# Kernel optimization log

Hardware: AMD Instinct MI355X
Metric: run time of the kernel (lower is better)

Reference implementation:

```python
import jax, jax.numpy as jnp
import numpy as np

H = 128   # hidden_size
C = 80    # number of classes / per-class GRUs


def setup_inputs():
    key = jax.random.key(0)
    ks = jax.random.split(key, 16)
    lengths = np.array([100 + 4 * j for j in range(C)], dtype=np.int64)   # ragged segment sizes
    ucl = np.concatenate([np.zeros(1, np.int64), np.cumsum(lengths)])     # [C+1] boundaries
    N = int(ucl[-1])                                                      # 20640 total boxes
    r = jax.random.normal
    return {
        "boxes_feature": r(ks[0], (N, 1024), jnp.float32),
        "boxes_score": r(ks[1], (N, 32), jnp.float32),
        "boxes_box": r(ks[2], (N, 4), jnp.float32),
        "all_class_boxes_feature": r(ks[3], (N, 1024), jnp.float32),
        "all_class_boxes_score": r(ks[4], (N, 32), jnp.float32),
        "all_class_boxes_box": r(ks[5], (N, 32), jnp.float32),
        "all_class_boxes_origin_score": r(ks[6], (N, 32), jnp.float32),
        "unique_class": np.ones(C, dtype=np.int64),
        "unique_class_len": ucl,
        "appear_W": r(ks[7], (H, 1024), jnp.float32) / np.sqrt(1024.0).astype(np.float32),
        "appear_b": jnp.zeros((H,), jnp.float32),
        "feat_W": r(ks[8], (H, H + 96), jnp.float32) / np.sqrt(float(H + 96)).astype(np.float32),
        "feat_b": jnp.zeros((H,), jnp.float32),
        "gru_Wih": r(ks[9], (C, 2, 3 * H, H), jnp.float32) / np.sqrt(float(H)).astype(np.float32),
        "gru_Whh": r(ks[10], (C, 2, 3 * H, H), jnp.float32) / np.sqrt(float(H)).astype(np.float32),
        "gru_bih": r(ks[11], (C, 2, 3 * H), jnp.float32) * 0.01,
        "gru_bhh": r(ks[12], (C, 2, 3 * H), jnp.float32) * 0.01,
        "out_W": r(ks[13], (1, 2 * H), jnp.float32) / np.sqrt(2.0 * H).astype(np.float32),
        "out_b": jnp.zeros((1,), jnp.float32),
    }


def _forward(all_class_boxes_feature, all_class_boxes_score, all_class_boxes_box,
             all_class_boxes_origin_score, unique_class, unique_class_len,
             appear_W, appear_b, feat_W, feat_b,
             gru_Wih, gru_Whh, gru_bih, gru_bhh, out_W, out_b):
    # --- static ragged bookkeeping (int inputs are concrete numpy) ---
    ucl = np.asarray(unique_class_len)
    lengths = ucl[1:] - ucl[:-1]                                   # [C]
    starts = ucl[:-1]
    L = int(lengths.max())
    t = np.arange(L)
    mask = jnp.asarray(t[None, :] < lengths[:, None])              # [C,L] valid-position mask
    gidx = jnp.asarray(starts[:, None] + np.minimum(t[None, :], lengths[:, None] - 1))  # [C,L]
    ridx = jnp.asarray(np.clip(lengths[:, None] - 1 - t[None, :], 0, None))             # [C,L]

    # --- shared feature pipeline ---
    feat = jax.nn.relu(all_class_boxes_feature @ appear_W.T + appear_b)   # [N,H]
    allf = jnp.concatenate([feat, all_class_boxes_score, all_class_boxes_box,
                            all_class_boxes_origin_score], axis=1)        # [N,H+96]
    dec = jax.nn.relu(allf @ feat_W.T + feat_b)                           # [N,H]

    X = dec[gidx]                                                  # [C,L,H] padded per-class segments
    Xr = jnp.take_along_axis(X, ridx[:, :, None], axis=1)          # time-reversed within each length

    def run_dir(Xd, Wih, Whh, bih, bhh):
        # precompute input projections; scan only carries the hidden recurrence
        Xp = jnp.einsum('clh,cgh->clg', Xd, Wih) + bih[:, None, :]  # [C,L,3H]

        def per_class(xp, m, Whh_c, bhh_c):
            def step(h, inp):
                x_t, m_t = inp
                gh = Whh_c @ h + bhh_c
                r = jax.nn.sigmoid(x_t[:H] + gh[:H])                # PyTorch gate order r,z,n
                z = jax.nn.sigmoid(x_t[H:2 * H] + gh[H:2 * H])
                n = jnp.tanh(x_t[2 * H:] + r * gh[2 * H:])
                h2 = jnp.where(m_t, (1.0 - z) * n + z * h, h)
                return h2, h2
            _, out = jax.lax.scan(step, jnp.zeros((H,), xp.dtype), (xp, m))
            return out                                              # [L,H]
        return jax.vmap(per_class)(Xp, mask, Whh, bhh)              # [C,L,H]

    out_f = run_dir(X, gru_Wih[:, 0], gru_Whh[:, 0], gru_bih[:, 0], gru_bhh[:, 0])
    out_r = run_dir(Xr, gru_Wih[:, 1], gru_Whh[:, 1], gru_bih[:, 1], gru_bhh[:, 1])
    out_bd = jnp.take_along_axis(out_r, ridx[:, :, None], axis=1)   # un-reverse backward outputs
    Y = jnp.concatenate([out_f, out_bd], axis=-1)                   # [C,L,2H]

    # flatten valid positions back to the original box order (segments are contiguous)
    seg = jnp.asarray(np.repeat(np.arange(C), lengths))
    loc = jnp.asarray(np.concatenate([np.arange(int(l)) for l in lengths]))
    flat = Y[seg, loc]                                              # [N,2H]
    return jax.nn.sigmoid(flat @ out_W.T + out_b)[:, None, :]       # [N,1,1] like torch output


def reference(boxes_feature, boxes_score, boxes_box, all_class_boxes_feature,
              all_class_boxes_score, all_class_boxes_box, all_class_boxes_origin_score,
              unique_class, unique_class_len, appear_W, appear_b, feat_W, feat_b,
              gru_Wih, gru_Whh, gru_bih, gru_bhh, out_W, out_b):
    # boxes_feature/boxes_score/boxes_box are accepted but unused, as in the torch forward
    return _forward(all_class_boxes_feature, all_class_boxes_score, all_class_boxes_box,
                    all_class_boxes_origin_score, unique_class, unique_class_len,
                    appear_W, appear_b, feat_W, feat_b,
                    gru_Wih, gru_Whh, gru_bih, gru_bhh, out_W, out_b)
```

## Files before the change

### kernel.cpp

```cpp
#include <hip/hip_runtime.h>
#include <hip/hip_bf16.h>
#include <cstdint>


typedef _Float16 half2_t __attribute__((ext_vector_type(2)));
typedef _Float16 half8_t __attribute__((ext_vector_type(8)));

__global__ __launch_bounds__(256) void concat_kernel(
    const float* __restrict__ score, const float* __restrict__ box,
    const float* __restrict__ orig, float* __restrict__ allf, int N)
{
    int idx = blockIdx.x * 256 + threadIdx.x;
    int total = N * 96;
    if (idx >= total) return;
    int n = idx / 96, j = idx - n * 96;
    float v;
    if (j < 32)      v = score[(size_t)n * 32 + j];
    else if (j < 64) v = box  [(size_t)n * 32 + j - 32];
    else             v = orig [(size_t)n * 32 + j - 64];
    allf[(size_t)n * 224 + 128 + j] = v;
}

__global__ __launch_bounds__(256) void gemm128_kernel(
    const float* __restrict__ A, int lda,
    const float* __restrict__ B,
    const float* __restrict__ bias,
    float* __restrict__ Cc, int ldc,
    int N, int K, int do_relu)
{
    __shared__ __align__(16) float As[16][64];
    __shared__ __align__(16) float Bs[16][128];
    const int tid = threadIdx.x;
    const int tx = tid & 15, ty = tid >> 4;
    const int n0 = blockIdx.x * 64;
    const int arow = tid >> 2;

    float acc[4][8] = {};

    int ar = n0 + arow; if (ar > N - 1) ar = N - 1;
    const float* Aptr  = A + (size_t)ar * lda + (tid & 3) * 4;
    const int m0 = tid >> 2;
    const int kq4 = (tid & 3) * 4;
    const float* Bptr0 = B + (size_t)m0 * K + (tid & 3) * 4;
    const float* Bptr1 = Bptr0 + (size_t)64 * K;

    float4 av = *(const float4*)(Aptr);
    float4 b0 = *(const float4*)(Bptr0);
    float4 b1 = *(const float4*)(Bptr1);

    for (int kb = 0; kb < K; kb += 16) {
        __syncthreads();
        As[kq4 + 0][arow] = av.x;
        As[kq4 + 1][arow] = av.y;
        As[kq4 + 2][arow] = av.z;
        As[kq4 + 3][arow] = av.w;
        Bs[kq4 + 0][m0] = b0.x; Bs[kq4 + 1][m0] = b0.y;
        Bs[kq4 + 2][m0] = b0.z; Bs[kq4 + 3][m0] = b0.w;
        Bs[kq4 + 0][m0 + 64] = b1.x; Bs[kq4 + 1][m0 + 64] = b1.y;
        Bs[kq4 + 2][m0 + 64] = b1.z; Bs[kq4 + 3][m0 + 64] = b1.w;
        __syncthreads();
        if (kb + 16 < K) {
            av = *(const float4*)(Aptr + kb + 16);
            b0 = *(const float4*)(Bptr0 + kb + 16);
            b1 = *(const float4*)(Bptr1 + kb + 16);
        }
        #pragma unroll
        for (int kk = 0; kk < 16; kk++) {
            float4 a = *(const float4*)&As[kk][ty * 4];
            float4 p = *(const float4*)&Bs[kk][tx * 8];
            float4 q = *(const float4*)&Bs[kk][tx * 8 + 4];
            float av4[4] = {a.x, a.y, a.z, a.w};
            float bv[8]  = {p.x, p.y, p.z, p.w, q.x, q.y, q.z, q.w};
            #pragma unroll
            for (int i = 0; i < 4; i++)
                #pragma unroll
                for (int j = 0; j < 8; j++)
                    acc[i][j] = fmaf(av4[i], bv[j], acc[i][j]);
        }
    }

    #pragma unroll
    for (int i = 0; i < 4; i++) {
        int row = n0 + ty * 4 + i;
        if (row >= N) continue;
        float o[8];
        #pragma unroll
        for (int j = 0; j < 8; j++) {
            float v = acc[i][j] + bias[tx * 8 + j];
            if (do_relu) v = v > 0.f ? v : 0.f;
            o[j] = v;
        }
        float4* dst = (float4*)(Cc + (size_t)row * ldc + tx * 8);
        dst[0] = make_float4(o[0], o[1], o[2], o[3]);
        dst[1] = make_float4(o[4], o[5], o[6], o[7]);
    }
}

__global__ __launch_bounds__(256) void xp_kernel(
    const float* __restrict__ dec,
    const float* __restrict__ Wih,
    const float* __restrict__ bih,
    const int* __restrict__ ucl,
    float* __restrict__ xp,
    int N)
{
    const int c = blockIdx.x;
    const int tile = blockIdx.y;
    const int d  = blockIdx.z / 3;
    const int mt = blockIdx.z % 3;
    const int start = ucl[c];
    const int len = ucl[c + 1] - start;
    const int t0 = tile * 64;
    if (t0 >= len) return;

    __shared__ __align__(16) float As[16][64];
    __shared__ __align__(16) float Bs[16][128];
    const int tid = threadIdx.x;
    const int tx = tid & 15, ty = tid >> 4;
    const int arow = tid >> 2;

    int t = t0 + arow; if (t > len - 1) t = len - 1;
    int srow = start + (d ? (len - 1 - t) : t);
    const float* Aptr = dec + (size_t)srow * 128 + (tid & 3) * 4;

    const float* Bbase = Wih + ((size_t)(c * 2 + d) * 384 + mt * 128) * 128;
    const int m0 = tid >> 2;
    const int kq4 = (tid & 3) * 4;
    const float* Bptr0 = Bbase + (size_t)m0 * 128 + (tid & 3) * 4;
    const float* Bptr1 = Bptr0 + (size_t)64 * 128;

    float4 av = *(const float4*)(Aptr);
    float4 b0 = *(const float4*)(Bptr0);
    float4 b1 = *(const float4*)(Bptr1);

    float acc[4][8] = {};
    for (int kb = 0; kb < 128; kb += 16) {
        __syncthreads();
        As[kq4 + 0][arow] = av.x;
        As[kq4 + 1][arow] = av.y;
        As[kq4 + 2][arow] = av.z;
        As[kq4 + 3][arow] = av.w;
        Bs[kq4 + 0][m0] = b0.x; Bs[kq4 + 1][m0] = b0.y;
        Bs[kq4 + 2][m0] = b0.z; Bs[kq4 + 3][m0] = b0.w;
        Bs[kq4 + 0][m0 + 64] = b1.x; Bs[kq4 + 1][m0 + 64] = b1.y;
        Bs[kq4 + 2][m0 + 64] = b1.z; Bs[kq4 + 3][m0 + 64] = b1.w;
        __syncthreads();
        if (kb + 16 < 128) {
            av = *(const float4*)(Aptr + kb + 16);
            b0 = *(const float4*)(Bptr0 + kb + 16);
            b1 = *(const float4*)(Bptr1 + kb + 16);
        }
        #pragma unroll
        for (int kk = 0; kk < 16; kk++) {
            float4 a = *(const float4*)&As[kk][ty * 4];
            float4 p = *(const float4*)&Bs[kk][tx * 8];
            float4 q = *(const float4*)&Bs[kk][tx * 8 + 4];
            float av4[4] = {a.x, a.y, a.z, a.w};
            float bv[8]  = {p.x, p.y, p.z, p.w, q.x, q.y, q.z, q.w};
            #pragma unroll
            for (int i = 0; i < 4; i++)
                #pragma unroll
                for (int j = 0; j < 8; j++)
                    acc[i][j] = fmaf(av4[i], bv[j], acc[i][j]);
        }
    }

    const float* bias = bih + (size_t)(c * 2 + d) * 384 + mt * 128;
    #pragma unroll
    for (int i = 0; i < 4; i++) {
        int tt = t0 + ty * 4 + i;
        if (tt >= len) continue;
        float o[8];
        #pragma unroll
        for (int j = 0; j < 8; j++) o[j] = acc[i][j] + bias[tx * 8 + j];
        float4* dst = (float4*)(xp + ((size_t)d * N + start + tt) * 384 + mt * 128 + tx * 8);
        dst[0] = make_float4(o[0], o[1], o[2], o[3]);
        dst[1] = make_float4(o[4], o[5], o[6], o[7]);
    }
}

__global__ __launch_bounds__(128, 1) void gru_kernel(
    const float* __restrict__ xp,
    const float* __restrict__ Whh,
    const float* __restrict__ bhh,
    const int* __restrict__ ucl,
    float* __restrict__ outY,
    int N)
{
    const int c = blockIdx.x, d = blockIdx.y;
    const int start = ucl[c];
    const int len = ucl[c + 1] - start;
    const int g = threadIdx.x;

    const float* wbase = Whh + (size_t)(c * 2 + d) * 384 * 128;
    half2_t w0[64], w1[64], w2[64];
    {
        const float2* r0 = (const float2*)(wbase + (size_t)g * 128);
        const float2* r1 = (const float2*)(wbase + (size_t)(g + 128) * 128);
        const float2* r2 = (const float2*)(wbase + (size_t)(g + 256) * 128);
        #pragma unroll
        for (int i = 0; i < 64; i++) {
            float2 a = r0[i];
            w0[i] = half2_t{(_Float16)a.x, (_Float16)a.y};
        }
        #pragma unroll
        for (int i = 0; i < 64; i++) {
            float2 a = r1[i];
            w1[i] = half2_t{(_Float16)a.x, (_Float16)a.y};
        }
        #pragma unroll
        for (int i = 0; i < 64; i++) {
            float2 a = r2[i];
            w2[i] = half2_t{(_Float16)a.x, (_Float16)a.y};
        }
    }
    const float* bb = bhh + (size_t)(c * 2 + d) * 384;
    const float bh0 = bb[g], bh1 = bb[g + 128], bh2 = bb[g + 256];

    __shared__ __align__(16) half2_t hbuf[2][64];
    if (g < 64) { hbuf[0][g] = half2_t{(_Float16)0.f, (_Float16)0.f}; }
    const float* xpb = xp + ((size_t)d * N + start) * 384;
    float* outb = outY + (size_t)start * 256 + d * 128;

    float x0 = xpb[g], x1 = xpb[g + 128], x2 = xpb[g + 256];
    float hcur = 0.f;
    __syncthreads();

    for (int t = 0; t < len; t++) {
        const half8_t* __restrict__ hp = (const half8_t*)hbuf[t & 1];
        _Float16* __restrict__ hn = (_Float16*)hbuf[(t & 1) ^ 1];
        float nx0 = 0.f, nx1 = 0.f, nx2 = 0.f;
        if (t + 1 < len) {
            const float* xr = xpb + (size_t)(t + 1) * 384;
            nx0 = xr[g]; nx1 = xr[g + 128]; nx2 = xr[g + 256];
        }
        float a0 = bh0, a1 = bh1, a2 = bh2;
        #pragma unroll
        for (int i = 0; i < 16; i++) {
            union { half8_t v; half2_t h2[4]; } u;
            u.v = hp[i];
            #pragma unroll
            for (int j = 0; j < 4; j++) {
                a0 = __builtin_amdgcn_fdot2(w0[i * 4 + j], u.h2[j], a0, false);
                a1 = __builtin_amdgcn_fdot2(w1[i * 4 + j], u.h2[j], a1, false);
                a2 = __builtin_amdgcn_fdot2(w2[i * 4 + j], u.h2[j], a2, false);
            }
        }
        float r = 1.f / (1.f + __expf(-(x0 + a0)));
        float z = 1.f / (1.f + __expf(-(x1 + a1)));
        float pre = x2 + r * a2;
        float n = 1.f - 2.f / (__expf(2.f * pre) + 1.f);
        float hnew = (1.f - z) * n + z * hcur;
        hn[g] = (_Float16)hnew;
        hcur = hnew;
        int tt = d ? (len - 1 - t) : t;
        outb[(size_t)tt * 256 + g] = hnew;
        x0 = nx0; x1 = nx1; x2 = nx2;
        __syncthreads();
    }
}

__global__ __launch_bounds__(256) void final_kernel(
    const float* __restrict__ outY,
    const float* __restrict__ outW,
    const float* __restrict__ outb,
    float* __restrict__ out, int N)
{
    __shared__ __align__(16) float wsh[256];
    wsh[threadIdx.x] = outW[threadIdx.x];
    __syncthreads();
    const int lane = threadIdx.x & 63;
    const int wave = (blockIdx.x * 256 + threadIdx.x) >> 6;
    const int nw = gridDim.x * 4;
    float4 w4 = *(const float4*)&wsh[lane * 4];
    float b = outb[0];
    for (int n = wave; n < N; n += nw) {
        float4 y = *(const float4*)(outY + (size_t)n * 256 + lane * 4);
        float p = y.x * w4.x + y.y * w4.y + y.z * w4.z + y.w * w4.w;
        #pragma unroll
        for (int off = 32; off > 0; off >>= 1) p += __shfl_down(p, off);
        if (lane == 0) out[n] = 1.f / (1.f + __expf(-(p + b)));
    }
}

extern "C" void kernel_launch(void* const* d_in, const int* in_sizes, int n_in,
                              void* d_out, int out_size, void* d_ws, size_t ws_size,
                              hipStream_t stream)
{
    const float* acbf  = (const float*)d_in[3];
    const float* score = (const float*)d_in[4];
    const float* box   = (const float*)d_in[5];
    const float* orig  = (const float*)d_in[6];
    const int*   ucl   = (const int*)d_in[8];
    const float* aW  = (const float*)d_in[9];
    const float* ab  = (const float*)d_in[10];
    const float* fW  = (const float*)d_in[11];
    const float* fb  = (const float*)d_in[12];
    const float* Wih = (const float*)d_in[13];
    const float* Whh = (const float*)d_in[14];
    const float* bih = (const float*)d_in[15];
    const float* bhh = (const float*)d_in[16];
    const float* oW  = (const float*)d_in[17];
    const float* ob  = (const float*)d_in[18];
    float* out = (float*)d_out;

    const int N = in_sizes[3] / 1024;
    const int C = in_sizes[7];

    float* ws   = (float*)d_ws;
    float* allf = ws;
    float* dec  = ws + (size_t)N * 224;
    float* xp   = dec + (size_t)N * 128;
    float* outY = ws;

    dim3 blk(256);
    concat_kernel<<<dim3((N * 96 + 255) / 256), blk, 0, stream>>>(score, box, orig, allf, N);
    gemm128_kernel<<<dim3((N + 63) / 64), blk, 0, stream>>>(acbf, 1024, aW, ab, allf, 224, N, 1024, 1);
    gemm128_kernel<<<dim3((N + 63) / 64), blk, 0, stream>>>(allf, 224, fW, fb, dec, 128, N, 224, 1);
    xp_kernel<<<dim3(C, 7, 6), blk, 0, stream>>>(dec, Wih, bih, ucl, xp, N);
    gru_kernel<<<dim3(C, 2), dim3(128), 0, stream>>>(xp, Whh, bhh, ucl, outY, N);
    final_kernel<<<dim3(160), blk, 0, stream>>>(outY, oW, ob, out, N);
}
```

Before: 715.6 us.

## Use lightweight LDS barriers and unroll GRU recurrence by two with deeper prefetch

Replaces __syncthreads with an inline-asm barrier that waits only on LDS/scalar counters (lgkmcnt) so outstanding global loads and stores need not drain at each barrier. The sequential GRU loop is unrolled by two with fixed ping-pong buffer indices and input projections prefetched two steps ahead, and the gate divides now use fast __fdividef. The aim is less per-timestep barrier and latency overhead on the serial critical path. The custom barrier relies on the compiler not reordering memory operations across it, and fast division slightly changes numerics.

New measurement: 715.8 us. Within noise of the previous version (+0.0%).

```diff
diff --git a/kernel.cpp b/kernel.cpp
--- a/kernel.cpp
+++ b/kernel.cpp
@@ -5,6 +5,10 @@
 
 typedef _Float16 half2_t __attribute__((ext_vector_type(2)));
 typedef _Float16 half8_t __attribute__((ext_vector_type(8)));
+
+__device__ __forceinline__ void lds_barrier() {
+    asm volatile("s_waitcnt lgkmcnt(0)\n\ts_barrier" ::: "memory");
+}
 
 __global__ __launch_bounds__(256) void concat_kernel(
     const float* __restrict__ score, const float* __restrict__ box,
@@ -49,7 +53,7 @@
     float4 b1 = *(const float4*)(Bptr1);
 
     for (int kb = 0; kb < K; kb += 16) {
-        __syncthreads();
+        lds_barrier();
         As[kq4 + 0][arow] = av.x;
         As[kq4 + 1][arow] = av.y;
         As[kq4 + 2][arow] = av.z;
@@ -58,7 +62,7 @@
         Bs[kq4 + 2][m0] = b0.z; Bs[kq4 + 3][m0] = b0.w;
         Bs[kq4 + 0][m0 + 64] = b1.x; Bs[kq4 + 1][m0 + 64] = b1.y;
         Bs[kq4 + 2][m0 + 64] = b1.z; Bs[kq4 + 3][m0 + 64] = b1.w;
-        __syncthreads();
+        lds_barrier();
         if (kb + 16 < K) {
             av = *(const float4*)(Aptr + kb + 16);
             b0 = *(const float4*)(Bptr0 + kb + 16);
@@ -135,7 +139,7 @@
 
     float acc[4][8] = {};
     for (int kb = 0; kb < 128; kb += 16) {
-        __syncthreads();
+        lds_barrier();
         As[kq4 + 0][arow] = av.x;
         As[kq4 + 1][arow] = av.y;
         As[kq4 + 2][arow] = av.z;
@@ -144,7 +148,7 @@
         Bs[kq4 + 2][m0] = b0.z; Bs[kq4 + 3][m0] = b0.w;
         Bs[kq4 + 0][m0 + 64] = b1.x; Bs[kq4 + 1][m0 + 64] = b1.y;
         Bs[kq4 + 2][m0 + 64] = b1.z; Bs[kq4 + 3][m0 + 64] = b1.w;
-        __syncthreads();
+        lds_barrier();
         if (kb + 16 < 128) {
             av = *(const float4*)(Aptr + kb + 16);
             b0 = *(const float4*)(Bptr0 + kb + 16);
@@ -222,42 +226,56 @@
     const float* xpb = xp + ((size_t)d * N + start) * 384;
     float* outb = outY + (size_t)start * 256 + d * 128;
 
-    float x0 = xpb[g], x1 = xpb[g + 128], x2 = xpb[g + 256];
+    float xa0 = xpb[g], xa1 = xpb[g + 128], xa2 = xpb[g + 256];
+    const size_t o1 = (size_t)((len > 1) ? 1 : 0) * 384;
+    float xb0 = xpb[o1 + g], xb1 = xpb[o1 + g + 128], xb2 = xpb[o1 + g + 256];
     float hcur = 0.f;
-    __syncthreads();
-
-    for (int t = 0; t < len; t++) {
-        const half8_t* __restrict__ hp = (const half8_t*)hbuf[t & 1];
-        _Float16* __restrict__ hn = (_Float16*)hbuf[(t & 1) ^ 1];
-        float nx0 = 0.f, nx1 = 0.f, nx2 = 0.f;
-        if (t + 1 < len) {
-            const float* xr = xpb + (size_t)(t + 1) * 384;
-            nx0 = xr[g]; nx1 = xr[g + 128]; nx2 = xr[g + 256];
-        }
-        float a0 = bh0, a1 = bh1, a2 = bh2;
-        #pragma unroll
-        for (int i = 0; i < 16; i++) {
-            union { half8_t v; half2_t h2[4]; } u;
-            u.v = hp[i];
-            #pragma unroll
-            for (int j = 0; j < 4; j++) {
-                a0 = __builtin_amdgcn_fdot2(w0[i * 4 + j], u.h2[j], a0, false);
-                a1 = __builtin_amdgcn_fdot2(w1[i * 4 + j], u.h2[j], a1, false);
-                a2 = __builtin_amdgcn_fdot2(w2[i * 4 + j], u.h2[j], a2, false);
-            }
-        }
-        float r = 1.f / (1.f + __expf(-(x0 + a0)));
-        float z = 1.f / (1.f + __expf(-(x1 + a1)));
-        float pre = x2 + r * a2;
-        float n = 1.f - 2.f / (__expf(2.f * pre) + 1.f);
-        float hnew = (1.f - z) * n + z * hcur;
-        hn[g] = (_Float16)hnew;
-        hcur = hnew;
-        int tt = d ? (len - 1 - t) : t;
-        outb[(size_t)tt * 256 + g] = hnew;
-        x0 = nx0; x1 = nx1; x2 = nx2;
-        __syncthreads();
-    }
+    lds_barrier();
+
+#define GRU_SUBSTEP(HP_IDX, HN_IDX, X0, X1, X2, TT)                          \
+    {                                                                        \
+        const half8_t* __restrict__ hp = (const half8_t*)hbuf[HP_IDX];       \
+        _Float16* __restrict__ hn = (_Float16*)hbuf[HN_IDX];                 \
+        float a0 = bh0, a1 = bh1, a2 = bh2;                                  \
+        _Pragma("unroll")                                                    \
+        for (int i = 0; i < 16; i++) {                                       \
+            union { half8_t v; half2_t h2[4]; } u;                           \
+            u.v = hp[i];                                                     \
+            _Pragma("unroll")                                                \
+            for (int j = 0; j < 4; j++) {                                    \
+                a0 = __builtin_amdgcn_fdot2(w0[i * 4 + j], u.h2[j], a0, false);\
+                a1 = __builtin_amdgcn_fdot2(w1[i * 4 + j], u.h2[j], a1, false);\
+                a2 = __builtin_amdgcn_fdot2(w2[i * 4 + j], u.h2[j], a2, false);\
+            }                                                                \
+        }                                                                    \
+        float r = __fdividef(1.f, 1.f + __expf(-((X0) + a0)));               \
+        float z = __fdividef(1.f, 1.f + __expf(-((X1) + a1)));               \
+        float pre = (X2) + r * a2;                                           \
+        float n = 1.f - __fdividef(2.f, __expf(2.f * pre) + 1.f);            \
+        float hnew = (1.f - z) * n + z * hcur;                               \
+        hn[g] = (_Float16)hnew;                                              \
+        hcur = hnew;                                                         \
+        outb[(size_t)(TT) * 256 + g] = hnew;                                 \
+    }
+
+    for (int t = 0; t < len; t += 2) {
+        int tpa = (t + 2 < len) ? (t + 2) : (len - 1);
+        const float* xra = xpb + (size_t)tpa * 384;
+        float ta0 = xra[g], ta1 = xra[g + 128], ta2 = xra[g + 256];
+        int ttA = d ? (len - 1 - t) : t;
+        GRU_SUBSTEP(0, 1, xa0, xa1, xa2, ttA)
+        xa0 = ta0; xa1 = ta1; xa2 = ta2;
+        lds_barrier();
+        if (t + 1 >= len) break;
+        int tpb = (t + 3 < len) ? (t + 3) : (len - 1);
+        const float* xrb = xpb + (size_t)tpb * 384;
+        float tb0 = xrb[g], tb1 = xrb[g + 128], tb2 = xrb[g + 256];
+        int ttB = d ? (len - 2 - t) : (t + 1);
+        GRU_SUBSTEP(1, 0, xb0, xb1, xb2, ttB)
+        xb0 = tb0; xb1 = tb1; xb2 = tb2;
+        lds_barrier();
+    }
+#undef GRU_SUBSTEP
 }
 
 __global__ __launch_bounds__(256) void final_kernel(
```
